# Performance work log

Hardware: AMD Instinct MI355X
Metric: run time of the kernel (lower is better)

Reference implementation:

```python
import jax, jax.numpy as jnp
import numpy as np

N, M, P = 32, 16, 32
B, T = 256, 200
STD_DYN, STD_OBS = 0.1, 0.1


def setup_inputs() -> dict:
    key = jax.random.key(0)
    k = jax.random.split(key, 6)
    Y = jax.random.normal(k[0], (B, T, P), dtype=jnp.float32)
    U = jax.random.normal(k[1], (B, T, M), dtype=jnp.float32)
    mask = jnp.ones((B, T), dtype=jnp.float32)
    # stable transition matrix
    A = 0.95 * jnp.eye(N, dtype=jnp.float32) + 0.05 * jax.random.normal(k[2], (N, N), dtype=jnp.float32) / np.sqrt(N)
    Bm = jax.random.normal(k[3], (N, M), dtype=jnp.float32) / np.sqrt(M)
    C = jax.random.normal(k[4], (P, N), dtype=jnp.float32) / np.sqrt(N)
    mu0 = jax.random.normal(k[5], (N,), dtype=jnp.float32)
    Sigma0 = jnp.eye(N, dtype=jnp.float32)
    Q = (STD_DYN ** 2) * jnp.eye(N, dtype=jnp.float32)
    R = (STD_OBS ** 2) * jnp.eye(P, dtype=jnp.float32)
    return {"Y": Y, "U": U, "mask": mask, "A": A, "Bm": Bm, "C": C,
            "mu0": mu0, "Sigma0": Sigma0, "Q": Q, "R": R}


def _sym(X):
    return 0.5 * (X + jnp.swapaxes(X, -1, -2))


def reference(Y, U, mask, A, Bm, C, mu0, Sigma0, Q, R):
    """Kalman filter forward pass (time-invariant A,B,C; Q,R diag buffers).
    Returns (mus_filt [B,T,n], Sigmas_filt [B,T,n,n], mus_pred [B,T,n],
             Sigmas_pred [B,T,n,n])."""
    Bsz = Y.shape[0]
    n = A.shape[0]
    I = jnp.eye(n, dtype=Y.dtype)

    mu_init = jnp.broadcast_to(mu0, (Bsz, n))                 # [B,n]
    Sig_init = jnp.broadcast_to(Sigma0, (Bsz, n, n))          # [B,n,n]

    def step(carry, inp):
        mu, Sigma = carry                                     # [B,n], [B,n,n]
        y_t, u_t, m_t = inp                                   # [B,p], [B,m], [B]
        # predict
        mu_pred = mu @ A.T + u_t @ Bm.T                       # [B,n]
        Sigma_pred = jnp.einsum('ij,bjk,lk->bil', A, Sigma, A) + Q
        # innovation
        r = y_t - mu_pred @ C.T                               # [B,p]
        S = _sym(jnp.einsum('ij,bjk,lk->bil', C, Sigma_pred, C) + R)  # [B,p,p]
        PCT = jnp.einsum('bij,kj->bik', Sigma_pred, C)        # [B,n,p]
        # gain: K = (solve(S, PCT^T))^T
        K = jnp.swapaxes(jnp.linalg.solve(S, jnp.swapaxes(PCT, -1, -2)), -1, -2)
        K = m_t[:, None, None] * K                            # mask missing obs
        # update (Joseph form)
        mu_new = mu_pred + jnp.einsum('bnp,bp->bn', K, r)
        I_KC = I - K @ C                                      # [B,n,n]
        Sigma_new = _sym(jnp.einsum('bij,bjk,blk->bil', I_KC, Sigma_pred, I_KC)
                         + jnp.einsum('bip,pq,bjq->bij', K, R, K))
        return (mu_new, Sigma_new), (mu_new, Sigma_new, mu_pred, Sigma_pred)

    xs = (jnp.swapaxes(Y, 0, 1), jnp.swapaxes(U, 0, 1), jnp.swapaxes(mask, 0, 1))
    _, (mf, Sf, mp, Sp) = jax.lax.scan(step, (mu_init, Sig_init), xs)
    # [T,B,...] -> [B,T,...]
    return (jnp.swapaxes(mf, 0, 1), jnp.swapaxes(Sf, 0, 1),
            jnp.swapaxes(mp, 0, 1), jnp.swapaxes(Sp, 0, 1))
```

## Files before the change

### kernel.cpp

```cpp
#include <hip/hip_runtime.h>
#include <math.h>

#define TT 200
#define ST 36
#define PA 33
#define FSTR 17

__device__ __forceinline__ float rdlane(float v, int l) {
  return __int_as_float(__builtin_amdgcn_readlane(__float_as_int(v), l));
}

#if __has_builtin(__builtin_amdgcn_rsqf)
#define RSQF(x) __builtin_amdgcn_rsqf(x)
#else
#define RSQF(x) (1.0f / sqrtf(x))
#endif

__device__ __forceinline__ float4 ld4(const float* p) { return *(const float4*)p; }
__device__ __forceinline__ void st4(float* p, float4 v) { *(float4*)p = v; }

__device__ __forceinline__ float dot32r(const float* __restrict__ row, const float (&a)[32]) {
  float s0 = 0.f, s1 = 0.f;
  #pragma unroll
  for (int k = 0; k < 32; k += 8) {
    float4 v0 = ld4(row + k);
    float4 v1 = ld4(row + k + 4);
    s0 = fmaf(a[k+0], v0.x, s0); s0 = fmaf(a[k+1], v0.y, s0);
    s0 = fmaf(a[k+2], v0.z, s0); s0 = fmaf(a[k+3], v0.w, s0);
    s1 = fmaf(a[k+4], v1.x, s1); s1 = fmaf(a[k+5], v1.y, s1);
    s1 = fmaf(a[k+6], v1.z, s1); s1 = fmaf(a[k+7], v1.w, s1);
  }
  return s0 + s1;
}

__device__ __forceinline__ void dot32x2(const float* __restrict__ row,
                                        const float (&a)[32], const float (&b)[32],
                                        float& oa, float& ob) {
  float a0=0.f, a1=0.f, b0=0.f, b1=0.f;
  #pragma unroll
  for (int k = 0; k < 32; k += 8) {
    float4 v0 = ld4(row + k);
    float4 v1 = ld4(row + k + 4);
    a0 = fmaf(a[k+0], v0.x, a0); a1 = fmaf(a[k+1], v0.y, a1);
    a0 = fmaf(a[k+2], v0.z, a0); a1 = fmaf(a[k+3], v0.w, a1);
    b0 = fmaf(b[k+0], v0.x, b0); b1 = fmaf(b[k+1], v0.y, b1);
    b0 = fmaf(b[k+2], v0.z, b0); b1 = fmaf(b[k+3], v0.w, b1);
    a0 = fmaf(a[k+4], v1.x, a0); a1 = fmaf(a[k+5], v1.y, a1);
    a0 = fmaf(a[k+6], v1.z, a0); a1 = fmaf(a[k+7], v1.w, a1);
    b0 = fmaf(b[k+4], v1.x, b0); b1 = fmaf(b[k+5], v1.y, b1);
    b0 = fmaf(b[k+6], v1.z, b0); b1 = fmaf(b[k+7], v1.w, b1);
  }
  oa = a0 + a1; ob = b0 + b1;
}

__device__ __forceinline__ void dot32x4(const float* __restrict__ row,
    const float (&a)[32], const float (&b)[32], const float (&c)[32], const float (&d)[32],
    float& oa, float& ob, float& oc, float& od) {
  float sa=0.f, sb=0.f, sc=0.f, sd=0.f;
  #pragma unroll
  for (int k = 0; k < 32; k += 4) {
    float4 v = ld4(row + k);
    sa = fmaf(a[k+0], v.x, sa); sb = fmaf(b[k+0], v.x, sb);
    sc = fmaf(c[k+0], v.x, sc); sd = fmaf(d[k+0], v.x, sd);
    sa = fmaf(a[k+1], v.y, sa); sb = fmaf(b[k+1], v.y, sb);
    sc = fmaf(c[k+1], v.y, sc); sd = fmaf(d[k+1], v.y, sd);
    sa = fmaf(a[k+2], v.z, sa); sb = fmaf(b[k+2], v.z, sb);
    sc = fmaf(c[k+2], v.z, sc); sd = fmaf(d[k+2], v.z, sd);
    sa = fmaf(a[k+3], v.w, sa); sb = fmaf(b[k+3], v.w, sb);
    sc = fmaf(c[k+3], v.w, sc); sd = fmaf(d[k+3], v.w, sd);
  }
  oa = sa; ob = sb; oc = sc; od = sd;
}

__device__ __forceinline__ float dot32rr(const float* __restrict__ ra, const float* __restrict__ rb) {
  float s0 = 0.f, s1 = 0.f;
  #pragma unroll
  for (int k = 0; k < 32; k += 8) {
    float4 x0 = ld4(ra + k), x1 = ld4(ra + k + 4);
    float4 y0 = ld4(rb + k), y1 = ld4(rb + k + 4);
    s0 = fmaf(x0.x, y0.x, s0); s0 = fmaf(x0.y, y0.y, s0);
    s0 = fmaf(x0.z, y0.z, s0); s0 = fmaf(x0.w, y0.w, s0);
    s1 = fmaf(x1.x, y1.x, s1); s1 = fmaf(x1.y, y1.y, s1);
    s1 = fmaf(x1.z, y1.z, s1); s1 = fmaf(x1.w, y1.w, s1);
  }
  return s0 + s1;
}

__global__ void __launch_bounds__(512, 2) kf_kernel(
    const float* __restrict__ Yg, const float* __restrict__ Ug,
    const float* __restrict__ Mg, const float* __restrict__ Ag,
    const float* __restrict__ Bg, const float* __restrict__ Cg,
    const float* __restrict__ mu0g, const float* __restrict__ S0g,
    const float* __restrict__ Qg, const float* __restrict__ Rg,
    float* __restrict__ out, int Bsz)
{
  __shared__ __align__(16) float SIG[32*ST];
  __shared__ __align__(16) float T1[32*ST];
  __shared__ __align__(16) float T1P[32*ST];
  __shared__ __align__(16) float SIGP[32*ST];
  __shared__ __align__(16) float T2T[33*ST];
  __shared__ __align__(16) float SR[32*ST];
  __shared__ __align__(16) float WT[33*ST];
  __shared__ __align__(16) float QL[1024];
  __shared__ __align__(16) float CQT[1024];
  __shared__ __align__(16) float EL[1024];
  __shared__ float ALDS[32*PA];
  __shared__ float DLDS[32*PA];
  __shared__ float FL[32*FSTR];
  __shared__ float u_lds[16], y_lds[32], mupred[32], mu_lds[32], mlds[2];

  const int tid = threadIdx.x;
  const int q = tid >> 5;
  const int r = tid & 31;
  const int b = blockIdx.x;
  const long btB = (long)b * TT;

  const long o_Sf = (long)Bsz * TT * 32;
  const long o_mp = o_Sf + (long)Bsz * TT * 32 * 32;
  const long o_Sp = o_mp + (long)Bsz * TT * 32;

  for (int e = tid; e < 1024; e += 512) {
    int i = e >> 5, k = e & 31;
    ALDS[i*PA + k] = Ag[e];
    SR[i*PA + k]   = Cg[e];
    QL[e] = Qg[e];
    SIG[i*ST + k] = S0g[e];
  }
  if (tid < 32) mu_lds[tid] = mu0g[tid];
  if (tid < 16) u_lds[tid] = Ug[btB*16 + tid];
  if (tid >= 64 && tid < 96) y_lds[tid-64] = Yg[btB*32 + (tid-64)];
  if (tid == 224) mlds[0] = Mg[btB];

  float aq0[32], aq1[32];
  #pragma unroll
  for (int k = 0; k < 32; k += 4) {
    float4 v;
    v = ld4(Ag + q*32 + k);      aq0[k]=v.x; aq0[k+1]=v.y; aq0[k+2]=v.z; aq0[k+3]=v.w;
    v = ld4(Ag + (q+16)*32 + k); aq1[k]=v.x; aq1[k+1]=v.y; aq1[k+2]=v.z; aq1[k+3]=v.w;
  }
  __syncthreads();

  {
    float d0 = 0.f, d1 = 0.f, x0 = 0.f, x1 = 0.f;
    #pragma unroll 8
    for (int k = 0; k < 32; ++k) {
      float al = ALDS[k*PA + r];
      d0 = fmaf(SR[q*PA + k],      al, d0);
      d1 = fmaf(SR[(q+16)*PA + k], al, d1);
      float cl = SR[r*PA + k];
      x0 = fmaf(cl, QL[k*32 + q],      x0);
      x1 = fmaf(cl, QL[k*32 + q + 16], x1);
    }
    DLDS[q*PA + r] = d0; DLDS[(q+16)*PA + r] = d1;
    CQT[q*32 + r] = x0;  CQT[(q+16)*32 + r] = x1;
    const int fi = tid >> 4, fj = tid & 15;
    float f = 0.f;
    #pragma unroll 8
    for (int k = 0; k < 32; ++k) f = fmaf(SR[fi*PA + k], Bg[k*16 + fj], f);
    FL[fi*FSTR + fj] = f;
  }
  __syncthreads();

  float dq0[32], dq1[32];
  {
    float e0 = 0.f, e1 = 0.f;
    #pragma unroll 8
    for (int k = 0; k < 32; ++k) {
      float cl = SR[r*PA + k];
      e0 = fmaf(CQT[k*32 + q],      cl, e0);
      e1 = fmaf(CQT[k*32 + q + 16], cl, e1);
    }
    EL[q*32 + r]      = e0 + Rg[q*32 + r];
    EL[(q+16)*32 + r] = e1 + Rg[(q+16)*32 + r];
    #pragma unroll
    for (int k = 0; k < 32; ++k) {
      dq0[k] = DLDS[q*PA + k];
      dq1[k] = DLDS[(q+16)*PA + k];
    }
  }
  __syncthreads();

  const int ro0 = q*ST + r;
  const int ro1 = (q+16)*ST + r;

  for (int t = 0; t < TT; ++t) {
    const long bt = btB + t;

    {
      float ta, tb, tc, td;
      dot32x4(SIG + r*ST, aq0, aq1, dq0, dq1, ta, tb, tc, td);
      T1[ro0] = ta; T1[ro1] = tb;
      T1P[ro0] = tc; T1P[ro1] = td;
      if (tid < 32) {
        float s = 0.f;
        #pragma unroll
        for (int k = 0; k < 32; ++k) s = fmaf(ALDS[tid*PA + k], mu_lds[k], s);
        #pragma unroll
        for (int k = 0; k < 16; ++k) s = fmaf(Bg[tid*16 + k], u_lds[k], s);
        mupred[tid] = s;
      } else if (tid >= 64 && tid < 96) {
        const int i = tid - 64;
        float s = y_lds[i];
        #pragma unroll
        for (int k = 0; k < 32; ++k) s = fmaf(-DLDS[i*PA + k], mu_lds[k], s);
        #pragma unroll
        for (int k = 0; k < 16; ++k) s = fmaf(-FL[i*FSTR + k], u_lds[k], s);
        T2T[32*ST + i] = s;
      }
    }
    __syncthreads();

    {
      float p0, p1;
      dot32x2(T1 + r*ST, aq0, aq1, p0, p1);
      float t2a, t2b, sa, sb;
      dot32x4(T1P + r*ST, aq0, aq1, dq0, dq1, t2a, t2b, sa, sb);
      SIGP[ro0] = p0 + QL[q*32 + r];
      SIGP[ro1] = p1 + QL[(q+16)*32 + r];
      T2T[ro0] = t2a + CQT[q*32 + r];
      T2T[ro1] = t2b + CQT[(q+16)*32 + r];
      SR[ro0] = sa + EL[q*32 + r];
      SR[ro1] = sb + EL[(q+16)*32 + r];
    }
    __syncthreads();

    if (tid < 64) {
      int cc = tid; if (cc > 32) cc = 32;
      float w[32], rr[32];
      #pragma unroll
      for (int kk = 0; kk < 32; kk += 4) {
        float4 vw = ld4(SR + cc*ST + kk);
        w[kk] = vw.x; w[kk+1] = vw.y; w[kk+2] = vw.z; w[kk+3] = vw.w;
        float4 vr = ld4(T2T + cc*ST + kk);
        rr[kk] = vr.x; rr[kk+1] = vr.y; rr[kk+2] = vr.z; rr[kk+3] = vr.w;
      }
      #pragma unroll
      for (int j = 0; j < 32; ++j) {
        float d  = rdlane(w[j], j);
        float sj = RSQF(d);
        float s2 = sj * sj;
        float gw = s2 * w[j];
        float gr = s2 * rr[j];
        WT[cc*ST + j] = rr[j] * sj;
        #pragma unroll
        for (int i = j+1; i < 32; ++i) {
          float bw = rdlane(w[i], j);
          w[i]  = fmaf(-bw, gw, w[i]);
          rr[i] = fmaf(-bw, gr, rr[i]);
        }
      }
    } else {
      const int u = tid - 64;
      if (u < 256) {
        st4(out + o_Sp + bt*1024 + u*4, ld4(SIGP + (u>>3)*ST + (u&7)*4));
      } else if (t > 0) {
        const int q2 = u - 256;
        st4(out + o_Sf + (bt-1)*1024 + q2*4, ld4(SIG + (q2>>3)*ST + (q2&7)*4));
      }
      if (u < 64 && t > 0) {
        const int q2 = u + 192;
        st4(out + o_Sf + (bt-1)*1024 + q2*4, ld4(SIG + (q2>>3)*ST + (q2&7)*4));
      }
      if (tid >= 64 && tid < 96)  out[o_mp + bt*32 + (tid-64)] = mupred[tid-64];
      if (t > 0 && tid >= 96 && tid < 128) out[(bt-1)*32 + (tid-96)] = mu_lds[tid-96];
      if (t < TT-1) {
        if (tid >= 128 && tid < 144) u_lds[tid-128] = Ug[(bt+1)*16 + (tid-128)];
        if (tid >= 160 && tid < 192) y_lds[tid-160] = Yg[(bt+1)*32 + (tid-160)];
        if (tid == 200) mlds[(t+1)&1] = Mg[bt+1];
      }
    }
    __syncthreads();

    {
      const float m = mlds[t&1];
      const float coefS = fmaf(m, m, -2.f*m);
      float rv[32];
      #pragma unroll
      for (int k = 0; k < 32; k += 4) {
        float4 v = ld4(WT + r*ST + k);
        rv[k] = v.x; rv[k+1] = v.y; rv[k+2] = v.z; rv[k+3] = v.w;
      }
      float ga = dot32r(WT + q*ST, rv);
      float gb = dot32r(WT + (q+16)*ST, rv);
      SIG[ro0] = fmaf(coefS, ga, SIGP[ro0]);
      SIG[ro1] = fmaf(coefS, gb, SIGP[ro1]);
      if (tid < 32) {
        float sacc = dot32rr(WT + tid*ST, WT + 32*ST);
        mu_lds[tid] = fmaf(m, sacc, mupred[tid]);
      }
    }
    __syncthreads();
  }

  {
    const long bt = btB + TT - 1;
    if (tid < 256)
      st4(out + o_Sf + bt*1024 + tid*4, ld4(SIG + (tid>>3)*ST + (tid&7)*4));
    if (tid >= 480)
      out[bt*32 + (tid - 480)] = mu_lds[tid - 480];
  }
}

extern "C" void kernel_launch(void* const* d_in, const int* in_sizes, int n_in,
                              void* d_out, int out_size, void* d_ws, size_t ws_size,
                              hipStream_t stream) {
  const float* Y   = (const float*)d_in[0];
  const float* U   = (const float*)d_in[1];
  const float* Mk  = (const float*)d_in[2];
  const float* A   = (const float*)d_in[3];
  const float* Bm  = (const float*)d_in[4];
  const float* C   = (const float*)d_in[5];
  const float* mu0 = (const float*)d_in[6];
  const float* S0  = (const float*)d_in[7];
  const float* Q   = (const float*)d_in[8];
  const float* R   = (const float*)d_in[9];
  int Bsz = in_sizes[2] / TT;
  kf_kernel<<<Bsz, 512, 0, stream>>>(Y, U, Mk, A, Bm, C, mu0, S0, Q, R,
                                     (float*)d_out, Bsz);
}
```

Before: 1.607 ms.

## Split Cholesky-style elimination across full wavefront and rebalance Sigma update

The triangular elimination that builds WT is reorganised so that each of the 64 lanes holds 16 rows instead of 32. Row j is broadcast with shuffles, and the extra column is carried in its own register array, rz, rather than through a spare lane. This halves the serial per-lane work in the critical path, at the cost of more cross-lane shuffles per step. The Sigma-filtered update is also remapped so 256 threads each compute a 2x2 output block, and a separate group of 32 threads handles the mean update concurrently.

```diff
diff --git a/kernel.cpp b/kernel.cpp
--- a/kernel.cpp
+++ b/kernel.cpp
@@ -225,28 +225,39 @@
     __syncthreads();
 
     if (tid < 64) {
-      int cc = tid; if (cc > 32) cc = 32;
-      float w[32], rr[32];
+      const int c  = tid & 31;
+      const int hb = tid >> 5;
+      const int side = hb << 5;
+      float w[16], rr[16], rz[16];
       #pragma unroll
-      for (int kk = 0; kk < 32; kk += 4) {
-        float4 vw = ld4(SR + cc*ST + kk);
-        w[kk] = vw.x; w[kk+1] = vw.y; w[kk+2] = vw.z; w[kk+3] = vw.w;
-        float4 vr = ld4(T2T + cc*ST + kk);
-        rr[kk] = vr.x; rr[kk+1] = vr.y; rr[kk+2] = vr.z; rr[kk+3] = vr.w;
+      for (int s4 = 0; s4 < 16; s4 += 2) {
+        float4 vw = ld4(SR  + c*ST  + s4*2);
+        float4 vr = ld4(T2T + c*ST  + s4*2);
+        float4 vz = ld4(T2T + 32*ST + s4*2);
+        w[s4]   = hb ? vw.y : vw.x;  w[s4+1]  = hb ? vw.w : vw.z;
+        rr[s4]  = hb ? vr.y : vr.x;  rr[s4+1] = hb ? vr.w : vr.z;
+        rz[s4]  = hb ? vz.y : vz.x;  rz[s4+1] = hb ? vz.w : vz.z;
       }
       #pragma unroll
       for (int j = 0; j < 32; ++j) {
-        float d  = rdlane(w[j], j);
-        float sj = RSQF(d);
-        float s2 = sj * sj;
-        float gw = s2 * w[j];
-        float gr = s2 * rr[j];
-        WT[cc*ST + j] = rr[j] * sj;
-        #pragma unroll
-        for (int i = j+1; i < 32; ++i) {
-          float bw = rdlane(w[i], j);
-          w[i]  = fmaf(-bw, gw, w[i]);
-          rr[i] = fmaf(-bw, gr, rr[i]);
+        const int pj = j & 1, sj = j >> 1;
+        float d   = rdlane(w[sj], j | (pj << 5));
+        float sjv = RSQF(d);
+        float s2  = sjv * sjv;
+        float mjw = __shfl(w[sj],  c | (pj << 5));
+        float mjr = __shfl(rr[sj], c | (pj << 5));
+        float mjz = __shfl(rz[sj], c | (pj << 5));
+        float gw = s2 * mjw, gr = s2 * mjr, gz = s2 * mjz;
+        if (hb == 0) {
+          WT[c*ST + j] = mjr * sjv;
+          if (c == 0) WT[32*ST + j] = mjz * sjv;
+        }
+        #pragma unroll
+        for (int s = sj; s < 16; ++s) {
+          float bw = __shfl(w[s], j + side);
+          w[s]  = fmaf(-bw, gw, w[s]);
+          rr[s] = fmaf(-bw, gr, rr[s]);
+          rz[s] = fmaf(-bw, gz, rz[s]);
         }
       }
     } else {
@@ -274,19 +285,28 @@
     {
       const float m = mlds[t&1];
       const float coefS = fmaf(m, m, -2.f*m);
-      float rv[32];
-      #pragma unroll
-      for (int k = 0; k < 32; k += 4) {
-        float4 v = ld4(WT + r*ST + k);
-        rv[k] = v.x; rv[k+1] = v.y; rv[k+2] = v.z; rv[k+3] = v.w;
-      }
-      float ga = dot32r(WT + q*ST, rv);
-      float gb = dot32r(WT + (q+16)*ST, rv);
-      SIG[ro0] = fmaf(coefS, ga, SIGP[ro0]);
-      SIG[ro1] = fmaf(coefS, gb, SIGP[ro1]);
-      if (tid < 32) {
-        float sacc = dot32rr(WT + tid*ST, WT + 32*ST);
-        mu_lds[tid] = fmaf(m, sacc, mupred[tid]);
+      if (tid < 256) {
+        const int qq = tid >> 4;
+        const int r2 = tid & 15;
+        float rv0[32], rv1[32];
+        #pragma unroll
+        for (int k = 0; k < 32; k += 4) {
+          float4 v0 = ld4(WT + r2*ST + k);
+          rv0[k]=v0.x; rv0[k+1]=v0.y; rv0[k+2]=v0.z; rv0[k+3]=v0.w;
+          float4 v1 = ld4(WT + (r2+16)*ST + k);
+          rv1[k]=v1.x; rv1[k+1]=v1.y; rv1[k+2]=v1.z; rv1[k+3]=v1.w;
+        }
+        float g00, g01, g10, g11;
+        dot32x2(WT + qq*ST,      rv0, rv1, g00, g01);
+        dot32x2(WT + (qq+16)*ST, rv0, rv1, g10, g11);
+        SIG[qq*ST + r2]          = fmaf(coefS, g00, SIGP[qq*ST + r2]);
+        SIG[qq*ST + r2 + 16]     = fmaf(coefS, g01, SIGP[qq*ST + r2 + 16]);
+        SIG[(qq+16)*ST + r2]     = fmaf(coefS, g10, SIGP[(qq+16)*ST + r2]);
+        SIG[(qq+16)*ST + r2 + 16]= fmaf(coefS, g11, SIGP[(qq+16)*ST + r2 + 16]);
+      } else if (tid < 288) {
+        const int i = tid - 256;
+        float sacc = dot32rr(WT + i*ST, WT + 32*ST);
+        mu_lds[i] = fmaf(m, sacc, mupred[i]);
       }
     }
     __syncthreads();
```

Result: slower. 5.387 ms (+235.3%).

## Move Sigma_pred computation off the critical path, overlapping it with Cholesky solve

Applied to the files above, without the earlier changes.

Moves the Sigma_pred = A·T1 + Q product out of the phase before the serial Cholesky-like elimination. Waves other than the first now compute it while wave 0 runs the elimination, and wave 0 computes its own share in the following phase. The Sigma_pred global store is deferred one step and handled by otherwise idle threads, with a final store added after the loop. This shortens the per-step critical path, at the cost of more complex bookkeeping for the deferred writes.

```diff
diff --git a/kernel.cpp b/kernel.cpp
--- a/kernel.cpp
+++ b/kernel.cpp
@@ -206,17 +206,16 @@
         #pragma unroll
         for (int k = 0; k < 16; ++k) s = fmaf(-FL[i*FSTR + k], u_lds[k], s);
         T2T[32*ST + i] = s;
+      } else if (t > 0 && tid >= 256) {
+        const int u2 = tid - 256;
+        st4(out + o_Sp + (bt-1)*1024 + u2*4, ld4(SIGP + (u2>>3)*ST + (u2&7)*4));
       }
     }
     __syncthreads();
 
     {
-      float p0, p1;
-      dot32x2(T1 + r*ST, aq0, aq1, p0, p1);
       float t2a, t2b, sa, sb;
       dot32x4(T1P + r*ST, aq0, aq1, dq0, dq1, t2a, t2b, sa, sb);
-      SIGP[ro0] = p0 + QL[q*32 + r];
-      SIGP[ro1] = p1 + QL[(q+16)*32 + r];
       T2T[ro0] = t2a + CQT[q*32 + r];
       T2T[ro1] = t2b + CQT[(q+16)*32 + r];
       SR[ro0] = sa + EL[q*32 + r];
@@ -250,17 +249,15 @@
         }
       }
     } else {
+      {
+        float p0, p1;
+        dot32x2(T1 + r*ST, aq0, aq1, p0, p1);
+        SIGP[ro0] = p0 + QL[q*32 + r];
+        SIGP[ro1] = p1 + QL[(q+16)*32 + r];
+      }
       const int u = tid - 64;
-      if (u < 256) {
-        st4(out + o_Sp + bt*1024 + u*4, ld4(SIGP + (u>>3)*ST + (u&7)*4));
-      } else if (t > 0) {
-        const int q2 = u - 256;
-        st4(out + o_Sf + (bt-1)*1024 + q2*4, ld4(SIG + (q2>>3)*ST + (q2&7)*4));
-      }
-      if (u < 64 && t > 0) {
-        const int q2 = u + 192;
-        st4(out + o_Sf + (bt-1)*1024 + q2*4, ld4(SIG + (q2>>3)*ST + (q2&7)*4));
-      }
+      if (t > 0 && u < 256)
+        st4(out + o_Sf + (bt-1)*1024 + u*4, ld4(SIG + (u>>3)*ST + (u&7)*4));
       if (tid >= 64 && tid < 96)  out[o_mp + bt*32 + (tid-64)] = mupred[tid-64];
       if (t > 0 && tid >= 96 && tid < 128) out[(bt-1)*32 + (tid-96)] = mu_lds[tid-96];
       if (t < TT-1) {
@@ -274,6 +271,17 @@
     {
       const float m = mlds[t&1];
       const float coefS = fmaf(m, m, -2.f*m);
+      float sp0, sp1;
+      if (tid < 64) {
+        dot32x2(T1 + r*ST, aq0, aq1, sp0, sp1);
+        sp0 += QL[q*32 + r];
+        sp1 += QL[(q+16)*32 + r];
+        SIGP[ro0] = sp0;
+        SIGP[ro1] = sp1;
+      } else {
+        sp0 = SIGP[ro0];
+        sp1 = SIGP[ro1];
+      }
       float rv[32];
       #pragma unroll
       for (int k = 0; k < 32; k += 4) {
@@ -282,8 +290,8 @@
       }
       float ga = dot32r(WT + q*ST, rv);
       float gb = dot32r(WT + (q+16)*ST, rv);
-      SIG[ro0] = fmaf(coefS, ga, SIGP[ro0]);
-      SIG[ro1] = fmaf(coefS, gb, SIGP[ro1]);
+      SIG[ro0] = fmaf(coefS, ga, sp0);
+      SIG[ro1] = fmaf(coefS, gb, sp1);
       if (tid < 32) {
         float sacc = dot32rr(WT + tid*ST, WT + 32*ST);
         mu_lds[tid] = fmaf(m, sacc, mupred[tid]);
@@ -296,6 +304,9 @@
     const long bt = btB + TT - 1;
     if (tid < 256)
       st4(out + o_Sf + bt*1024 + tid*4, ld4(SIG + (tid>>3)*ST + (tid&7)*4));
+    else
+      st4(out + o_Sp + bt*1024 + (tid-256)*4,
+          ld4(SIGP + ((tid-256)>>3)*ST + ((tid-256)&7)*4));
     if (tid >= 480)
       out[bt*32 + (tid - 480)] = mu_lds[tid - 480];
   }
```

Measured after the change: 1.916 ms. 19.2% more time.
